# Kernel optimization log

Measured on AMD Instinct MI355X. Metric: run time of the kernel, lower is better.

## Reference

```python
import jax, jax.numpy as jnp
import numpy as np

D = 1024
H = 16
HD = D // H
T = 2048
B = 2
EPS = 1e-6


def rmsnorm(x, w):
    xf = x.astype(jnp.float32)
    n = xf * jax.lax.rsqrt(jnp.mean(xf * xf, axis=-1, keepdims=True) + EPS)
    return n.astype(x.dtype) * w


def setup_inputs() -> dict:
    key = jax.random.key(0)
    ks = jax.random.split(key, 12)
    s_in = 1.0 / np.sqrt(D)
    s_h = 1.0 / np.sqrt(HD * H)
    s_ff = 1.0 / np.sqrt(4 * D)
    return {
        "x": jax.random.normal(ks[0], (B, T, D), jnp.float32),
        "wq": jax.random.normal(ks[1], (H, D, HD), jnp.float32) * s_in,
        "wk": jax.random.normal(ks[2], (H, D, HD), jnp.float32) * s_in,
        "wv": jax.random.normal(ks[3], (H, D, HD), jnp.float32) * s_in,
        "w_proj": jax.random.normal(ks[4], (D, D), jnp.float32) * s_h,
        "b_proj": jax.random.normal(ks[5], (D,), jnp.float32) * 0.01,
        "w1": jax.random.normal(ks[6], (D, 8 * D), jnp.float32) * s_in,
        "b1": jax.random.normal(ks[7], (8 * D,), jnp.float32) * 0.01,
        "w2": jax.random.normal(ks[8], (4 * D, D), jnp.float32) * s_ff,
        "b2": jax.random.normal(ks[9], (D,), jnp.float32) * 0.01,
        "g1": jnp.ones((D,), jnp.float32),
        "g2": jnp.ones((D,), jnp.float32),
    }


def reference(x, wq, wk, wv, w_proj, b_proj, w1, b1, w2, b2, g1, g2):
    # --- attention sub-block ---
    xn = rmsnorm(x, g1)
    q = jnp.einsum("btd,hde->bhte", xn, wq)  # [B,H,T,HD]
    k = jnp.einsum("btd,hde->bhte", xn, wk)
    v = jnp.einsum("btd,hde->bhte", xn, wv)
    scores = jnp.einsum("bhte,bhse->bhts", q, k) * (HD ** -0.5)
    causal = jnp.tril(jnp.ones((T, T), bool))
    scores = jnp.where(causal, scores, -jnp.inf)
    attn = jax.nn.softmax(scores, axis=-1)
    o = jnp.einsum("bhts,bhse->bhte", attn, v)  # [B,H,T,HD]
    o = o.transpose(0, 2, 1, 3).reshape(B, T, H * HD)  # concat heads
    x = x + o @ w_proj + b_proj
    # --- GLU FFN sub-block ---
    xn2 = rmsnorm(x, g2)
    h = xn2 @ w1 + b1  # [B,T,8D]
    a, b = jnp.split(h, 2, axis=-1)
    glu = a * jax.nn.sigmoid(b)  # [B,T,4D]
    x = x + glu @ w2 + b2
    return x
```

## Files before the change

### kernel.cpp

```cpp
#include <hip/hip_runtime.h>


typedef __attribute__((ext_vector_type(4))) float f32x4;
typedef __attribute__((ext_vector_type(8))) short short8;

typedef __attribute__((address_space(1))) const void gvoid;
typedef __attribute__((address_space(3))) void lvoid;

static __device__ __forceinline__ void gl_lds16(const void* g, void* l) {
  __builtin_amdgcn_global_load_lds((gvoid*)g, (lvoid*)l, 16, 0, 0);
}

static __device__ __forceinline__ unsigned short f2bf(float f) {
  union { float f; unsigned u; } v; v.f = f;
  unsigned r = v.u + 0x7fffu + ((v.u >> 16) & 1u);
  return (unsigned short)(r >> 16);
}
static __device__ __forceinline__ float to_f32(float v) { return v; }
static __device__ __forceinline__ float to_f32(unsigned short v) {
  union { unsigned u; float f; } x; x.u = ((unsigned)v) << 16; return x.f;
}

static __device__ __forceinline__ f32x4 mfma16(short8 a, short8 b, f32x4 c) {
  return __builtin_amdgcn_mfma_f32_16x16x32_bf16(a, b, c, 0, 0, 0);
}

template <typename Tin>
__global__ __launch_bounds__(256) void transpose_cvt(
    const Tin* __restrict__ in, unsigned short* __restrict__ out,
    int in_ld, long in_bstride, int out_ld, long out_bstride)
{
  __shared__ float tile[64][65];
  const Tin* inp = in + (long)blockIdx.z * in_bstride;
  unsigned short* outp = out + (long)blockIdx.z * out_bstride;
  int r0 = blockIdx.y * 64, c0 = blockIdx.x * 64;
  int tx = threadIdx.x & 63, ty = threadIdx.x >> 6;
#pragma unroll
  for (int i = ty; i < 64; i += 4)
    tile[i][tx] = to_f32(inp[(long)(r0 + i) * in_ld + (c0 + tx)]);
  __syncthreads();
#pragma unroll
  for (int i = ty; i < 64; i += 4)
    outp[(long)(c0 + i) * out_ld + (r0 + tx)] = f2bf(tile[tx][i]);
}

__global__ __launch_bounds__(256) void qkvw_repack(
    const float* __restrict__ wq, const float* __restrict__ wk,
    const float* __restrict__ wv, unsigned short* __restrict__ out)
{
  __shared__ float tile[64][65];
  const int z = blockIdx.z, head = z & 15, src = z >> 4;
  const float* inp = (src == 0 ? wq : src == 1 ? wk : wv) + (long)head * 1024 * 64;
  unsigned short* outp = out + ((long)src * 1024 + head * 64) * 1024;
  int r0 = blockIdx.y * 64;
  int tx = threadIdx.x & 63, ty = threadIdx.x >> 6;
#pragma unroll
  for (int i = ty; i < 64; i += 4)
    tile[i][tx] = inp[(long)(r0 + i) * 64 + tx];
  __syncthreads();
#pragma unroll
  for (int i = ty; i < 64; i += 4)
    outp[(long)i * 1024 + r0 + tx] = f2bf(tile[tx][i]);
}

__global__ __launch_bounds__(256) void rmsnorm_k(
    const float* __restrict__ x, const float* __restrict__ g,
    unsigned short* __restrict__ out)
{
  int row = blockIdx.x;
  int t = threadIdx.x;
  float4 v = ((const float4*)(x + (long)row * 1024))[t];
  float ss = v.x * v.x + v.y * v.y + v.z * v.z + v.w * v.w;
#pragma unroll
  for (int ofs = 32; ofs; ofs >>= 1) ss += __shfl_down(ss, ofs);
  __shared__ float red[4];
  if ((t & 63) == 0) red[t >> 6] = ss;
  __syncthreads();
  float sc = rsqrtf((red[0] + red[1] + red[2] + red[3]) * (1.0f / 1024.0f) + 1e-6f);
  float4 gv = ((const float4*)g)[t];
  ushort4 o4;
  o4.x = f2bf(v.x * sc * gv.x); o4.y = f2bf(v.y * sc * gv.y);
  o4.z = f2bf(v.z * sc * gv.z); o4.w = f2bf(v.w * sc * gv.w);
  ((ushort4*)(out + (long)row * 1024))[t] = o4;
}

template <int EPI, int BM, int BK, int WM_, int WN_, bool GLUB>
__global__ __launch_bounds__(256, 2) void gemm_bt(
    const unsigned short* __restrict__ A, const unsigned short* __restrict__ Bt,
    unsigned short* __restrict__ outb, float* __restrict__ outf,
    const float* __restrict__ res, const float* __restrict__ bias,
    int K, int lda, int ldbt, int ldout)
{
  constexpr int FM = BM / (16 * WM_);
  constexpr int FN = 128 / (16 * WN_);
  constexpr int KK = BK / 32;
  constexpr int UR = BK / 8;
  constexpr int ARn = BM * UR / 256;
  constexpr int BRn = 128 * UR / 256;
  __shared__ alignas(16) unsigned short Asm_[BM * BK];
  __shared__ alignas(16) unsigned short Bsm_[128 * BK];
  const int tid = threadIdx.x, lane = tid & 63, wave = tid >> 6;
  const int lr = lane & 15, lg = lane >> 4;
  const int wr = wave / WN_, wc = wave % WN_;
  const int m0 = blockIdx.y * BM;

  f32x4 acc[FM][FN];
#pragma unroll
  for (int mi = 0; mi < FM; mi++)
#pragma unroll
    for (int ni = 0; ni < FN; ni++) acc[mi][ni] = f32x4{0.f, 0.f, 0.f, 0.f};

  int rr_[BRn], ru_[BRn];
  long brow[BRn];
#pragma unroll
  for (int i = 0; i < BRn; i++) {
    int U = tid + 256 * i;
    int r = U / UR, u = U % UR;
    rr_[i] = r;
    ru_[i] = ((u & ~7) | ((u ^ r) & 7)) * 8;
    if (GLUB)
      brow[i] = (r < 64) ? (long)(blockIdx.x * 64 + r)
                         : (long)(4096 + blockIdx.x * 64 + r - 64);
    else
      brow[i] = (long)blockIdx.x * 128 + r;
  }

  for (int k0 = 0; k0 < K; k0 += BK) {
#pragma unroll
    for (int i = 0; i < BRn; i++) {
      if (i < ARn)
        gl_lds16(A + (long)(m0 + rr_[i]) * lda + k0 + ru_[i],
                 (char*)Asm_ + (tid + 256 * i) * 16);
      gl_lds16(Bt + brow[i] * ldbt + k0 + ru_[i],
               (char*)Bsm_ + (tid + 256 * i) * 16);
    }
    __syncthreads();

    short8 af[FM][KK], bfr[FN][KK];
#pragma unroll
    for (int mi = 0; mi < FM; mi++) {
      int row = wr * 16 * FM + mi * 16 + lr;
#pragma unroll
      for (int kk = 0; kk < KK; kk++) {
        int u = kk * 4 + lg;
        int off = row * (2 * BK) + ((u & ~7) | ((u ^ (row & 7)) & 7)) * 16;
        af[mi][kk] = *(const short8*)((const char*)Asm_ + off);
      }
    }
#pragma unroll
    for (int ni = 0; ni < FN; ni++) {
      int row = wc * 16 * FN + ni * 16 + lr;
#pragma unroll
      for (int kk = 0; kk < KK; kk++) {
        int u = kk * 4 + lg;
        int off = row * (2 * BK) + ((u & ~7) | ((u ^ (row & 7)) & 7)) * 16;
        bfr[ni][kk] = *(const short8*)((const char*)Bsm_ + off);
      }
    }
#pragma unroll
    for (int kk = 0; kk < KK; kk++)
#pragma unroll
      for (int mi = 0; mi < FM; mi++)
#pragma unroll
        for (int ni = 0; ni < FN; ni++)
          acc[mi][ni] = mfma16(af[mi][kk], bfr[ni][kk], acc[mi][ni]);
    __syncthreads();
  }

  const int rb = m0 + wr * 16 * FM + 4 * lg;
  if constexpr (EPI == 0) {
#pragma unroll
    for (int mi = 0; mi < FM; mi++)
#pragma unroll
      for (int ni = 0; ni < FN; ni++) {
        int col = blockIdx.x * 128 + wc * 16 * FN + ni * 16 + lr;
#pragma unroll
        for (int r = 0; r < 4; r++)
          outb[(long)(rb + mi * 16 + r) * ldout + col] = f2bf(acc[mi][ni][r]);
      }
  } else if constexpr (EPI == 1) {
#pragma unroll
    for (int mi = 0; mi < FM; mi++)
#pragma unroll
      for (int ni = 0; ni < FN; ni++) {
        int col = blockIdx.x * 128 + wc * 16 * FN + ni * 16 + lr;
        float bv = bias[col];
#pragma unroll
        for (int r = 0; r < 4; r++) {
          long idx = (long)(rb + mi * 16 + r) * ldout + col;
          outf[idx] = acc[mi][ni][r] + res[idx] + bv;
        }
      }
  } else {
#pragma unroll
    for (int mi = 0; mi < FM; mi++)
#pragma unroll
      for (int ni = 0; ni < FN / 2; ni++) {
        int col = blockIdx.x * 64 + ni * 16 + lr;
        float ba = bias[col], bb2 = bias[4096 + col];
#pragma unroll
        for (int r = 0; r < 4; r++) {
          float a = acc[mi][ni][r] + ba;
          float b = acc[mi][ni + FN / 2][r] + bb2;
          float s = 1.0f / (1.0f + __expf(-b));
          outb[(long)(rb + mi * 16 + r) * ldout + col] = f2bf(a * s);
        }
      }
  }
}

__global__ __launch_bounds__(256, 2) void attn_k(
    const unsigned short* __restrict__ qkv, const unsigned short* __restrict__ vt,
    unsigned short* __restrict__ o)
{
  __shared__ alignas(16) unsigned short Ksm[2 * 128 * 64];
  __shared__ alignas(16) unsigned short Vsm[2 * 64 * 128];
  __shared__ alignas(16) unsigned short Psm[4][16 * 128];
  const int tid = threadIdx.x, lane = tid & 63, wave = tid >> 6;
  const int lr = lane & 15, lg = lane >> 4;
  const int bh = blockIdx.y, b = bh >> 4, h = bh & 15;
  const int ia = blockIdx.x;
  const int tA0 = ia * 64, tB0 = (31 - ia) * 64;
  const int nchA = (ia + 2) >> 1, nchB = (33 - ia) >> 1;
  const float NEGINF = -__builtin_inff();

  short8 qfA[2], qfB[2];
  {
    const unsigned short* qp =
        qkv + (long)(b * 2048 + tA0 + wave * 16 + lr) * 3072 + h * 64 + lg * 8;
    qfA[0] = *(const short8*)qp;  qfA[1] = *(const short8*)(qp + 32);
    qp = qkv + (long)(b * 2048 + tB0 + wave * 16 + lr) * 3072 + h * 64 + lg * 8;
    qfB[0] = *(const short8*)qp;  qfB[1] = *(const short8*)(qp + 32);
  }
  f32x4 oA[4], oB[4];
#pragma unroll
  for (int n = 0; n < 4; n++) { oA[n] = f32x4{0,0,0,0}; oB[n] = f32x4{0,0,0,0}; }
  float mA = NEGINF, lA = 0.f, mB = NEGINF, lB = 0.f;

  const long kbase = (long)(b * 2048) * 3072 + 1024 + h * 64;
  const long vbase = (long)bh * 64 * 2048;

  auto stage = [&](int buf, int c) {
    const int s0 = c * 128;
#pragma unroll
    for (int i = 0; i < 4; i++) {
      int U = tid + 256 * i;
      int kr = U >> 3, ku = (U ^ kr) & 7;
      gl_lds16(qkv + kbase + (long)(s0 + kr) * 3072 + ku * 8,
               (char*)Ksm + (buf * 1024 + wave * 64 + 256 * i) * 16);
      int vr = U >> 4, vu = (U & 8) | ((U ^ vr) & 7);
      gl_lds16(vt + vbase + (long)vr * 2048 + s0 + vu * 8,
               (char*)Vsm + (buf * 1024 + wave * 64 + 256 * i) * 16);
    }
  };

  char* pb = (char*)&Psm[wave][0];

  auto process = [&](const short8* qf, f32x4* o_acc, float& m, float& l,
                     const char* kb, const char* vb, int s0, int qg, bool diag) {
    f32x4 s[8];
#pragma unroll
    for (int n = 0; n < 8; n++) s[n] = f32x4{0.f, 0.f, 0.f, 0.f};
    __builtin_amdgcn_s_setprio(1);
#pragma unroll
    for (int n = 0; n < 8; n++) {
      int row = n * 16 + lr;
#pragma unroll
      for (int kk = 0; kk < 2; kk++) {
        int off = row * 128 + (((kk * 4 + lg) ^ row) & 7) * 16;
        short8 kf = *(const short8*)(kb + off);
        s[n] = mfma16(kf, qf[kk], s[n]);
      }
    }
    __builtin_amdgcn_s_setprio(0);
#pragma unroll
    for (int n = 0; n < 8; n++)
#pragma unroll
      for (int r = 0; r < 4; r++) {
        float v = s[n][r] * 0.125f;
        if (diag && (s0 + n * 16 + 4 * lg + r > qg)) v = NEGINF;
        s[n][r] = v;
      }
    float t[8];
#pragma unroll
    for (int n = 0; n < 8; n++)
      t[n] = fmaxf(fmaxf(s[n][0], s[n][1]), fmaxf(s[n][2], s[n][3]));
    float mx = fmaxf(fmaxf(fmaxf(t[0], t[1]), fmaxf(t[2], t[3])),
                     fmaxf(fmaxf(t[4], t[5]), fmaxf(t[6], t[7])));
    mx = fmaxf(mx, __shfl_xor(mx, 16));
    mx = fmaxf(mx, __shfl_xor(mx, 32));
    if (!__all(mx <= m + 8.0f)) {
      float mn = fmaxf(m, mx);
      float alpha = __expf(m - mn);
      m = mn;
      l *= alpha;
#pragma unroll
      for (int r = 0; r < 4; r++) {
        float ar = __shfl(alpha, 4 * lg + r);
#pragma unroll
        for (int n = 0; n < 4; n++) o_acc[n][r] *= ar;
      }
    }
    float sum = 0.f;
#pragma unroll
    for (int n = 0; n < 8; n++)
#pragma unroll
      for (int r = 0; r < 4; r++) {
        float p = __expf(s[n][r] - m);
        s[n][r] = p;
        sum += p;
      }
    sum += __shfl_xor(sum, 16);
    sum += __shfl_xor(sum, 32);
    l += sum;
#pragma unroll
    for (int n = 0; n < 8; n++) {
      unsigned lo = (unsigned)f2bf(s[n][0]) | ((unsigned)f2bf(s[n][1]) << 16);
      unsigned hi = (unsigned)f2bf(s[n][2]) | ((unsigned)f2bf(s[n][3]) << 16);
      int u = 2 * n + (lg >> 1);
      int su = (u & 8) | ((u ^ lr) & 7);
      *(uint2*)(pb + lr * 256 + su * 16 + 8 * (lg & 1)) = uint2{lo, hi};
    }
    asm volatile("s_waitcnt lgkmcnt(0)" ::: "memory");
    __builtin_amdgcn_sched_barrier(0);
    short8 pa[4];
#pragma unroll
    for (int ks = 0; ks < 4; ks++) {
      int u = 4 * ks + lg;
      int su = (u & 8) | ((u ^ lr) & 7);
      pa[ks] = *(const short8*)(pb + lr * 256 + su * 16);
    }
    __builtin_amdgcn_s_setprio(1);
#pragma unroll
    for (int n = 0; n < 4; n++) {
      int row = n * 16 + lr;
#pragma unroll
      for (int ks = 0; ks < 4; ks++) {
        int u = 4 * ks + lg;
        int su = (u & 8) | ((u ^ row) & 7);
        short8 vf = *(const short8*)(vb + row * 256 + su * 16);
        o_acc[n] = mfma16(pa[ks], vf, o_acc[n]);
      }
    }
    __builtin_amdgcn_s_setprio(0);
  };

  stage(0, 0);
  __syncthreads();

  const int qgA = tA0 + wave * 16 + lr, qgB = tB0 + wave * 16 + lr;
  for (int c = 0; c < nchB; c++) {
    if (c + 1 < nchB) stage((c + 1) & 1, c + 1);
    const char* kb = (const char*)Ksm + (c & 1) * 16384;
    const char* vb = (const char*)Vsm + (c & 1) * 16384;
    const int s0 = c * 128;
    if (c < nchA) process(qfA, oA, mA, lA, kb, vb, s0, qgA, c == nchA - 1);
    process(qfB, oB, mB, lB, kb, vb, s0, qgB, c == nchB - 1);
    __syncthreads();
  }

  auto finish = [&](const f32x4* o_acc, float l, int t0) {
#pragma unroll
    for (int r = 0; r < 4; r++) {
      float inv = 1.0f / __shfl(l, 4 * lg + r);
      int trow = t0 + wave * 16 + 4 * lg + r;
#pragma unroll
      for (int n = 0; n < 4; n++)
        o[(long)(b * 2048 + trow) * 1024 + h * 64 + n * 16 + lr] =
            f2bf(o_acc[n][r] * inv);
    }
  };
  finish(oA, lA, tA0);
  finish(oB, lB, tB0);
}

extern "C" void kernel_launch(void* const* d_in, const int* in_sizes, int n_in,
                              void* d_out, int out_size, void* d_ws, size_t ws_size,
                              hipStream_t stream) {
  const float* x     = (const float*)d_in[0];
  const float* wq    = (const float*)d_in[1];
  const float* wk    = (const float*)d_in[2];
  const float* wv    = (const float*)d_in[3];
  const float* wproj = (const float*)d_in[4];
  const float* bproj = (const float*)d_in[5];
  const float* w1    = (const float*)d_in[6];
  const float* b1    = (const float*)d_in[7];
  const float* w2    = (const float*)d_in[8];
  const float* b2    = (const float*)d_in[9];
  const float* g1    = (const float*)d_in[10];
  const float* g2    = (const float*)d_in[11];
  (void)in_sizes; (void)n_in; (void)out_size; (void)ws_size;

  char* ws = (char*)d_ws;
  unsigned short* wt_qkv = (unsigned short*)(ws);
  unsigned short* wpt    = (unsigned short*)(ws + (6ul << 20));
  unsigned short* w1t    = (unsigned short*)(ws + (8ul << 20));
  unsigned short* w2t    = (unsigned short*)(ws + (24ul << 20));
  unsigned short* xn     = (unsigned short*)(ws + (32ul << 20));
  unsigned short* qkv    = (unsigned short*)(ws + (40ul << 20));
  unsigned short* vt     = (unsigned short*)(ws + (64ul << 20));
  unsigned short* glu    = (unsigned short*)(ws + (40ul << 20));
  unsigned short* obuf   = (unsigned short*)(ws + (72ul << 20));
  float*          x1     = (float*)(ws + (80ul << 20));
  float* outf = (float*)d_out;

  qkvw_repack<<<dim3(1, 16, 48), 256, 0, stream>>>(wq, wk, wv, wt_qkv);
  transpose_cvt<float><<<dim3(16, 16, 1), 256, 0, stream>>>(
      wproj, wpt, 1024, 0, 1024, 0);
  transpose_cvt<float><<<dim3(128, 16, 1), 256, 0, stream>>>(
      w1, w1t, 8192, 0, 1024, 0);
  transpose_cvt<float><<<dim3(16, 64, 1), 256, 0, stream>>>(
      w2, w2t, 1024, 0, 4096, 0);

  rmsnorm_k<<<4096, 256, 0, stream>>>(x, g1, xn);

  gemm_bt<0, 128, 64, 2, 2, false><<<dim3(24, 32), 256, 0, stream>>>(
      xn, wt_qkv, qkv, nullptr, nullptr, nullptr, 1024, 1024, 1024, 3072);

  transpose_cvt<unsigned short><<<dim3(1, 32, 16), 256, 0, stream>>>(
      qkv + 2048, vt, 3072, 64, 2048, (long)64 * 2048);
  transpose_cvt<unsigned short><<<dim3(1, 32, 16), 256, 0, stream>>>(
      qkv + 2048ul * 3072 + 2048, vt + 16ul * 64 * 2048, 3072, 64, 2048, (long)64 * 2048);

  attn_k<<<dim3(16, 32), 256, 0, stream>>>(qkv, vt, obuf);

  gemm_bt<1, 64, 128, 2, 2, false><<<dim3(8, 64), 256, 0, stream>>>(
      obuf, wpt, nullptr, x1, x, bproj, 1024, 1024, 1024, 1024);

  rmsnorm_k<<<4096, 256, 0, stream>>>(x1, g2, xn);

  gemm_bt<2, 128, 64, 4, 1, true><<<dim3(64, 32), 256, 0, stream>>>(
      xn, w1t, glu, nullptr, nullptr, b1, 1024, 1024, 1024, 4096);

  gemm_bt<1, 64, 128, 2, 2, false><<<dim3(8, 64), 256, 0, stream>>>(
      glu, w2t, nullptr, outf, x1, b2, 4096, 4096, 4096, 1024);
}
```

Measured before the change: 286.5 us.

## Merge weight repack and V-transpose launches; interleave QK MFMAs across query groups

All four weight repack/transpose launches are folded into one 4096-block kernel that picks its source by block index. The two per-batch V transposes become one 2D-grid kernel. In attention, the QK^T MFMAs for both query groups are issued back to back at raised priority before either softmax/PV stage runs. The goal is fewer kernel launches and tail bubbles, plus more MFMA work in flight, at the cost of extra live registers for two score tiles.

```diff
diff --git a/kernel.cpp b/kernel.cpp
--- a/kernel.cpp
+++ b/kernel.cpp
@@ -25,42 +25,63 @@
   return __builtin_amdgcn_mfma_f32_16x16x32_bf16(a, b, c, 0, 0, 0);
 }
 
-template <typename Tin>
-__global__ __launch_bounds__(256) void transpose_cvt(
-    const Tin* __restrict__ in, unsigned short* __restrict__ out,
-    int in_ld, long in_bstride, int out_ld, long out_bstride)
+__global__ __launch_bounds__(256) void repack_all(
+    const float* __restrict__ wq, const float* __restrict__ wk,
+    const float* __restrict__ wv, const float* __restrict__ wproj,
+    const float* __restrict__ w1, const float* __restrict__ w2,
+    unsigned short* __restrict__ wt_qkv, unsigned short* __restrict__ wpt,
+    unsigned short* __restrict__ w1t, unsigned short* __restrict__ w2t)
 {
   __shared__ float tile[64][65];
-  const Tin* inp = in + (long)blockIdx.z * in_bstride;
-  unsigned short* outp = out + (long)blockIdx.z * out_bstride;
-  int r0 = blockIdx.y * 64, c0 = blockIdx.x * 64;
+  const int bid = blockIdx.x;
+  const float* in;
+  unsigned short* out;
+  int r0, c0, in_ld, out_ld;
+  if (bid < 768) {
+    int z = bid >> 4, y = bid & 15;
+    int head = z & 15, src = z >> 4;
+    in = (src == 0 ? wq : src == 1 ? wk : wv) + (long)head * 1024 * 64;
+    out = wt_qkv + ((long)src * 1024 + head * 64) * 1024;
+    r0 = y * 64; c0 = 0; in_ld = 64; out_ld = 1024;
+  } else if (bid < 1024) {
+    int f = bid - 768;
+    in = wproj; out = wpt;
+    c0 = (f & 15) * 64; r0 = (f >> 4) * 64; in_ld = 1024; out_ld = 1024;
+  } else if (bid < 3072) {
+    int f = bid - 1024;
+    in = w1; out = w1t;
+    c0 = (f & 127) * 64; r0 = (f >> 7) * 64; in_ld = 8192; out_ld = 1024;
+  } else {
+    int f = bid - 3072;
+    in = w2; out = w2t;
+    c0 = (f & 15) * 64; r0 = (f >> 4) * 64; in_ld = 1024; out_ld = 4096;
+  }
   int tx = threadIdx.x & 63, ty = threadIdx.x >> 6;
 #pragma unroll
   for (int i = ty; i < 64; i += 4)
-    tile[i][tx] = to_f32(inp[(long)(r0 + i) * in_ld + (c0 + tx)]);
+    tile[i][tx] = in[(long)(r0 + i) * in_ld + (c0 + tx)];
   __syncthreads();
 #pragma unroll
   for (int i = ty; i < 64; i += 4)
-    outp[(long)(c0 + i) * out_ld + (r0 + tx)] = f2bf(tile[tx][i]);
-}
-
-__global__ __launch_bounds__(256) void qkvw_repack(
-    const float* __restrict__ wq, const float* __restrict__ wk,
-    const float* __restrict__ wv, unsigned short* __restrict__ out)
+    out[(long)(c0 + i) * out_ld + (r0 + tx)] = f2bf(tile[tx][i]);
+}
+
+__global__ __launch_bounds__(256) void vt_repack(
+    const unsigned short* __restrict__ qkv, unsigned short* __restrict__ vt)
 {
   __shared__ float tile[64][65];
-  const int z = blockIdx.z, head = z & 15, src = z >> 4;
-  const float* inp = (src == 0 ? wq : src == 1 ? wk : wv) + (long)head * 1024 * 64;
-  unsigned short* outp = out + ((long)src * 1024 + head * 64) * 1024;
-  int r0 = blockIdx.y * 64;
+  const int bh = blockIdx.y, b = bh >> 4, h = bh & 15;
+  const unsigned short* in = qkv + (long)b * 2048 * 3072 + 2048 + h * 64;
+  unsigned short* out = vt + (long)bh * 64 * 2048;
+  int r0 = blockIdx.x * 64;
   int tx = threadIdx.x & 63, ty = threadIdx.x >> 6;
 #pragma unroll
   for (int i = ty; i < 64; i += 4)
-    tile[i][tx] = inp[(long)(r0 + i) * 64 + tx];
+    tile[i][tx] = to_f32(in[(long)(r0 + i) * 3072 + tx]);
   __syncthreads();
 #pragma unroll
   for (int i = ty; i < 64; i += 4)
-    outp[(long)i * 1024 + r0 + tx] = f2bf(tile[tx][i]);
+    out[(long)i * 2048 + (r0 + tx)] = f2bf(tile[tx][i]);
 }
 
 __global__ __launch_bounds__(256) void rmsnorm_k(
@@ -256,12 +277,9 @@
 
   char* pb = (char*)&Psm[wave][0];
 
-  auto process = [&](const short8* qf, f32x4* o_acc, float& m, float& l,
-                     const char* kb, const char* vb, int s0, int qg, bool diag) {
-    f32x4 s[8];
+  auto qk = [&](const short8* qf, f32x4* s, const char* kb) {
 #pragma unroll
     for (int n = 0; n < 8; n++) s[n] = f32x4{0.f, 0.f, 0.f, 0.f};
-    __builtin_amdgcn_s_setprio(1);
 #pragma unroll
     for (int n = 0; n < 8; n++) {
       int row = n * 16 + lr;
@@ -272,7 +290,10 @@
         s[n] = mfma16(kf, qf[kk], s[n]);
       }
     }
-    __builtin_amdgcn_s_setprio(0);
+  };
+
+  auto smpv = [&](f32x4* s, f32x4* o_acc, float& m, float& l,
+                  const char* vb, int s0, int qg, bool diag) {
 #pragma unroll
     for (int n = 0; n < 8; n++)
 #pragma unroll
@@ -354,8 +375,14 @@
     const char* kb = (const char*)Ksm + (c & 1) * 16384;
     const char* vb = (const char*)Vsm + (c & 1) * 16384;
     const int s0 = c * 128;
-    if (c < nchA) process(qfA, oA, mA, lA, kb, vb, s0, qgA, c == nchA - 1);
-    process(qfB, oB, mB, lB, kb, vb, s0, qgB, c == nchB - 1);
+    const bool doA = (c < nchA);
+    f32x4 sA[8], sB[8];
+    __builtin_amdgcn_s_setprio(1);
+    if (doA) qk(qfA, sA, kb);
+    qk(qfB, sB, kb);
+    __builtin_amdgcn_s_setprio(0);
+    if (doA) smpv(sA, oA, mA, lA, vb, s0, qgA, c == nchA - 1);
+    smpv(sB, oB, mB, lB, vb, s0, qgB, c == nchB - 1);
     __syncthreads();
   }
 
@@ -404,23 +431,15 @@
   float*          x1     = (float*)(ws + (80ul << 20));
   float* outf = (float*)d_out;
 
-  qkvw_repack<<<dim3(1, 16, 48), 256, 0, stream>>>(wq, wk, wv, wt_qkv);
-  transpose_cvt<float><<<dim3(16, 16, 1), 256, 0, stream>>>(
-      wproj, wpt, 1024, 0, 1024, 0);
-  transpose_cvt<float><<<dim3(128, 16, 1), 256, 0, stream>>>(
-      w1, w1t, 8192, 0, 1024, 0);
-  transpose_cvt<float><<<dim3(16, 64, 1), 256, 0, stream>>>(
-      w2, w2t, 1024, 0, 4096, 0);
+  repack_all<<<4096, 256, 0, stream>>>(wq, wk, wv, wproj, w1, w2,
+                                       wt_qkv, wpt, w1t, w2t);
 
   rmsnorm_k<<<4096, 256, 0, stream>>>(x, g1, xn);
 
   gemm_bt<0, 128, 64, 2, 2, false><<<dim3(24, 32), 256, 0, stream>>>(
       xn, wt_qkv, qkv, nullptr, nullptr, nullptr, 1024, 1024, 1024, 3072);
 
-  transpose_cvt<unsigned short><<<dim3(1, 32, 16), 256, 0, stream>>>(
-      qkv + 2048, vt, 3072, 64, 2048, (long)64 * 2048);
-  transpose_cvt<unsigned short><<<dim3(1, 32, 16), 256, 0, stream>>>(
-      qkv + 2048ul * 3072 + 2048, vt + 16ul * 64 * 2048, 3072, 64, 2048, (long)64 * 2048);
+  vt_repack<<<dim3(32, 32), 256, 0, stream>>>(qkv, vt);
 
   attn_k<<<dim3(16, 32), 256, 0, stream>>>(qkv, vt, obuf);
 
```

New measurement: 270.0 us. -5.8%, faster.
